# Kernel tuning notes

Hardware: AMD Instinct MI355X
Metric: run time of the kernel (lower is better)

The kernel has to match this reference:

```python
import jax, jax.numpy as jnp
import numpy as np

B, S, H = 16, 512, 2048
NH, NKV = 16, 4
HD = H // NH  # 128


def _rope_tables(seq_len, dim, dtype):
    inv_freq = 1.0 / (10000.0 ** (jnp.arange(0, dim, 2, dtype=jnp.float32) / dim))
    t = jnp.arange(seq_len, dtype=jnp.float32)
    freqs = jnp.einsum('i,j->ij', t, inv_freq)          # [S, HD/2]
    emb = jnp.concatenate([freqs, freqs], axis=-1)       # [S, HD]
    cos = jnp.cos(emb)[None, None].astype(dtype)         # [1,1,S,HD]
    sin = jnp.sin(emb)[None, None].astype(dtype)
    return cos, sin


def _rotate_half(x):
    x1, x2 = jnp.split(x, 2, axis=-1)
    return jnp.concatenate([-x2, x1], axis=-1)


def setup_inputs() -> dict:
    key = jax.random.key(0)
    kx, kq, kk, kv, ko = jax.random.split(key, 5)
    x = jax.random.normal(kx, (B, S, H), dtype=jnp.float32)
    s = 0.02
    Wq = jax.random.normal(kq, (H, H), dtype=jnp.float32) * s
    Wk = jax.random.normal(kk, (NKV * HD, H), dtype=jnp.float32) * s
    Wv = jax.random.normal(kv, (NKV * HD, H), dtype=jnp.float32) * s
    Wo = jax.random.normal(ko, (H, H), dtype=jnp.float32) * s
    return {"x": x, "Wq": Wq, "Wk": Wk, "Wv": Wv, "Wo": Wo}


def reference(x, Wq, Wk, Wv, Wo):
    b, s, _ = x.shape
    scaling = HD ** -0.5
    # projections (torch Linear: y = x @ W.T, W is [out,in])
    q = jnp.einsum('bsh,oh->bso', x, Wq).reshape(b, s, NH, HD).transpose(0, 2, 1, 3)
    k = jnp.einsum('bsh,oh->bso', x, Wk).reshape(b, s, NKV, HD).transpose(0, 2, 1, 3)
    v = jnp.einsum('bsh,oh->bso', x, Wv).reshape(b, s, NKV, HD).transpose(0, 2, 1, 3)
    cos, sin = _rope_tables(s, HD, x.dtype)
    q = q * cos + _rotate_half(q) * sin
    k = k * cos + _rotate_half(k) * sin
    rep = NH // NKV
    k = jnp.repeat(k, rep, axis=1)  # [b, NH, s, HD]
    v = jnp.repeat(v, rep, axis=1)
    scores = jnp.einsum('bhqd,bhkd->bhqk', q, k) * scaling
    attn = jax.nn.softmax(scores, axis=-1)
    out = jnp.einsum('bhqk,bhkd->bhqd', attn, v)
    out = out.transpose(0, 2, 1, 3).reshape(b, s, H)
    return jnp.einsum('bsh,oh->bso', out, Wo)
```

## Files before the change

### kernel.cpp

```cpp
#include <hip/hip_runtime.h>
#include <stdint.h>


typedef _Float16 f16;
typedef _Float16 f16x4 __attribute__((ext_vector_type(4)));
typedef _Float16 f16x8 __attribute__((ext_vector_type(8)));
typedef float f32x4 __attribute__((ext_vector_type(4)));

#define B_   16
#define S_   512
#define H_   2048
#define NH_  16
#define NKV_ 4
#define HD_  128
#define ATT_SCALE 0.08838834764831843f
#define LOG2_10000_DIV64 0.20762050593045952f

#define AS1 __attribute__((address_space(1)))
#define AS3 __attribute__((address_space(3)))

__device__ __forceinline__ void async16(const void* g, const void* l) {
  __builtin_amdgcn_global_load_lds((const AS1 unsigned int*)(uintptr_t)g,
                                   (AS3 unsigned int*)(uintptr_t)l, 16, 0, 0);
}

__global__ __launch_bounds__(256) void cast_all(const float* __restrict__ x,
                                                const float* __restrict__ wq,
                                                const float* __restrict__ wk,
                                                const float* __restrict__ wv,
                                                const float* __restrict__ wo,
                                                f16* __restrict__ x_h,
                                                f16* __restrict__ w_h,
                                                f16* __restrict__ wo_h) {
  const int i = blockIdx.x * 256 + threadIdx.x;
  const float4* src;
  f16x4* dst;
  if (i < 4194304) {
    src = (const float4*)x + i;            dst = (f16x4*)x_h + i;
  } else if (i < 5242880) {
    int j = i - 4194304;
    src = (const float4*)wq + j;           dst = (f16x4*)w_h + j;
  } else if (i < 5505024) {
    int j = i - 5242880;
    src = (const float4*)wk + j;           dst = (f16x4*)w_h + 1048576 + j;
  } else if (i < 5767168) {
    int j = i - 5505024;
    src = (const float4*)wv + j;           dst = (f16x4*)w_h + 1310720 + j;
  } else {
    int j = i - 5767168;
    src = (const float4*)wo + j;           dst = (f16x4*)wo_h + j;
  }
  float4 v = *src;
  f16x4 o = {(f16)v.x, (f16)v.y, (f16)v.z, (f16)v.w};
  *dst = o;
}

template<int MODE>
__global__ __launch_bounds__(512, 2) void gemm_k(const f16* __restrict__ A,
                                                 const f16* __restrict__ W,
                                                 f16* __restrict__ qo,
                                                 f16* __restrict__ ko,
                                                 f16* __restrict__ vto,
                                                 float* __restrict__ fout) {
  __shared__ __align__(16) f16 As[3][256 * 64];
  __shared__ __align__(16) f16 Bs[3][128 * 64];
  const int K = 2048;
  const int NT = 32;
  const int m0 = blockIdx.x * 256;
  const int n0 = blockIdx.y * 128;
  const int tid = threadIdx.x;
  const int wave = tid >> 6, lane = tid & 63;
  const int quad = lane >> 4, l15 = lane & 15;
  const int wm = wave >> 1, wn = wave & 1;

  const f16* aptr[4];
  const f16* bptr[2];
#pragma unroll
  for (int i = 0; i < 4; ++i) {
    const int L = i * 512 + wave * 64 + lane;
    const int r = L >> 3, s = L & 7;
    aptr[i] = A + (size_t)(m0 + r) * K + (s ^ (r & 7)) * 8;
  }
#pragma unroll
  for (int i = 0; i < 2; ++i) {
    const int L = i * 512 + wave * 64 + lane;
    const int r = L >> 3, s = L & 7;
    bptr[i] = W + (size_t)(n0 + r) * K + (s ^ (r & 7)) * 8;
  }
  const int ldsw = wave * 1024;

  f32x4 acc[4][4] = {};
  f16x8 aC[4], bC[4], aN[4], bN[4];

  auto ldA = [&](f16x8* d, const f16* base, int ks) {
#pragma unroll
    for (int mi = 0; mi < 4; ++mi) {
      const int row = wm * 64 + mi * 16 + l15;
      const int slot = (ks * 4 + quad) ^ (l15 & 7);
      d[mi] = *reinterpret_cast<const f16x8*>(base + row * 64 + slot * 8);
    }
  };
  auto ldB = [&](f16x8* d, const f16* base, int ks) {
#pragma unroll
    for (int ni = 0; ni < 4; ++ni) {
      const int col = wn * 32 + (ni >> 1) * 64 + (ni & 1) * 16 + l15;
      const int slot = (ks * 4 + quad) ^ (l15 & 7);
      d[ni] = *reinterpret_cast<const f16x8*>(base + col * 64 + slot * 8);
    }
  };
  auto mfma16 = [&](const f16x8* Af, const f16x8* Bf) {
#pragma unroll
    for (int mi = 0; mi < 4; ++mi)
#pragma unroll
      for (int ni = 0; ni < 4; ++ni)
        acc[mi][ni] = __builtin_amdgcn_mfma_f32_16x16x32_f16(Af[mi], Bf[ni], acc[mi][ni], 0, 0, 0);
  };

#pragma unroll
  for (int t = 0; t < 2; ++t) {
#pragma unroll
    for (int i = 0; i < 4; ++i)
      async16(aptr[i] + t * 64, (const char*)&As[t][0] + i * 8192 + ldsw);
#pragma unroll
    for (int i = 0; i < 2; ++i)
      async16(bptr[i] + t * 64, (const char*)&Bs[t][0] + i * 8192 + ldsw);
  }
  asm volatile("s_waitcnt vmcnt(6)" ::: "memory");
  __builtin_amdgcn_s_barrier();
  ldA(aC, &As[0][0], 0);
  ldB(bC, &Bs[0][0], 0);

  for (int t = 0; t < NT; ++t) {
    const int buf = t % 3, bufn = (t + 1) % 3, bufs = (t + 2) % 3;
    const int sk = (t + 2) * 64;

    ldA(aN, &As[buf][0], 1);
    ldB(bN, &Bs[buf][0], 1);
    if (t + 2 < NT) {
      async16(aptr[0] + sk, (const char*)&As[bufs][0] + 0 * 8192 + ldsw);
      async16(aptr[1] + sk, (const char*)&As[bufs][0] + 1 * 8192 + ldsw);
      async16(bptr[0] + sk, (const char*)&Bs[bufs][0] + 0 * 8192 + ldsw);
    }
    asm volatile("s_waitcnt lgkmcnt(8)" ::: "memory");
    __builtin_amdgcn_sched_barrier(0);
    __builtin_amdgcn_s_setprio(1);
    mfma16(aC, bC);
    __builtin_amdgcn_s_setprio(0);

    if (t + 1 < NT) {
      if (t + 2 < NT) asm volatile("s_waitcnt vmcnt(3)" ::: "memory");
      else            asm volatile("s_waitcnt vmcnt(0)" ::: "memory");
      __builtin_amdgcn_s_barrier();
    }

    if (t + 1 < NT) {
      ldA(aC, &As[bufn][0], 0);
      ldB(bC, &Bs[bufn][0], 0);
    }
    if (t + 2 < NT) {
      async16(aptr[2] + sk, (const char*)&As[bufs][0] + 2 * 8192 + ldsw);
      async16(aptr[3] + sk, (const char*)&As[bufs][0] + 3 * 8192 + ldsw);
      async16(bptr[1] + sk, (const char*)&Bs[bufs][0] + 1 * 8192 + ldsw);
    }
    if (t + 1 < NT) asm volatile("s_waitcnt lgkmcnt(8)" ::: "memory");
    else            asm volatile("s_waitcnt lgkmcnt(0)" ::: "memory");
    __builtin_amdgcn_sched_barrier(0);
    __builtin_amdgcn_s_setprio(1);
    mfma16(aN, bN);
    __builtin_amdgcn_s_setprio(0);
    if (t + 1 < NT) __builtin_amdgcn_s_barrier();
  }

  if constexpr (MODE == 1) {
    const int b_ = m0 >> 9;
    if (n0 >= 2560) {
      const int h = (n0 - 2560) >> 7;
      f16* vb = vto + ((size_t)b_ * NKV_ + h) * HD_ * S_;
#pragma unroll
      for (int mi = 0; mi < 4; ++mi)
#pragma unroll
        for (int r = 0; r < 4; ++r) {
          const int s = (m0 + wm * 64 + mi * 16 + quad * 4 + r) & 511;
#pragma unroll
          for (int ni = 0; ni < 4; ++ni) {
            const int d = (ni >> 1) * 64 + wn * 32 + (ni & 1) * 16 + l15;
            vb[(size_t)d * S_ + s] = (f16)acc[mi][ni][r];
          }
        }
    } else {
      f16* ob = (n0 < 2048)
          ? (qo + ((size_t)b_ * NH_ + (n0 >> 7)) * S_ * HD_)
          : (ko + ((size_t)b_ * NKV_ + ((n0 - 2048) >> 7)) * S_ * HD_);
      float invf[2];
#pragma unroll
      for (int ni = 0; ni < 2; ++ni)
        invf[ni] = exp2f((float)(wn * 32 + ni * 16 + l15) * -LOG2_10000_DIV64);
#pragma unroll
      for (int mi = 0; mi < 4; ++mi)
#pragma unroll
        for (int r = 0; r < 4; ++r) {
          const int s = (m0 + wm * 64 + mi * 16 + quad * 4 + r) & 511;
          const size_t rb = (size_t)s * HD_;
#pragma unroll
          for (int ni = 0; ni < 2; ++ni) {
            const int d = wn * 32 + ni * 16 + l15;
            float sn, cs;
            __sincosf((float)s * invf[ni], &sn, &cs);
            const float x1 = acc[mi][ni][r], x2 = acc[mi][ni + 2][r];
            ob[rb + d] = (f16)(x1 * cs - x2 * sn);
            ob[rb + d + 64] = (f16)(x2 * cs + x1 * sn);
          }
        }
    }
  } else {
#pragma unroll
    for (int mi = 0; mi < 4; ++mi)
#pragma unroll
      for (int ni = 0; ni < 4; ++ni) {
        const int ncol = n0 + wn * 32 + (ni >> 1) * 64 + (ni & 1) * 16 + l15;
#pragma unroll
        for (int r = 0; r < 4; ++r) {
          const int mrow = m0 + wm * 64 + mi * 16 + quad * 4 + r;
          fout[(size_t)mrow * 2048 + ncol] = acc[mi][ni][r];
        }
      }
  }
}

__global__ __launch_bounds__(512) void attn_kernel(const f16* __restrict__ q,
                                                   const f16* __restrict__ k,
                                                   const f16* __restrict__ vt,
                                                   f16* __restrict__ out) {
  __shared__ __align__(16) f16 Qs[128 * 128];
  __shared__ __align__(16) f16 Ks[128 * 128];
  __shared__ __align__(16) f16 Vs[128 * 128];
  __shared__ __align__(16) f16 Ps[8][16 * 136];

  const int qt = blockIdx.x, h = blockIdx.y, b = blockIdx.z;
  const int kvh = h >> 2;
  const int tid = threadIdx.x;
  const int wave = tid >> 6, lane = tid & 63;
  const int quad = lane >> 4, l15 = lane & 15;
  const int sm0 = wave * 16;

  const f16* qbase = q + (((size_t)b * NH_ + h) * S_ + qt * 128) * HD_;
  const f16* kbase = k + ((size_t)b * NKV_ + kvh) * S_ * HD_;
  const f16* vbase = vt + ((size_t)b * NKV_ + kvh) * HD_ * S_;

#pragma unroll
  for (int i = 0; i < 4; ++i) {
    const int L = wave * 256 + i * 64 + lane;
    const int r = L >> 4;
    const int c = (L & 15) ^ (r & 15);
    async16(qbase + (size_t)r * HD_ + c * 8, (const char*)Qs + (size_t)(wave * 256 + i * 64) * 16);
  }

  f32x4 O[8] = {};
  float mrun[4], lrun[4];
#pragma unroll
  for (int r = 0; r < 4; ++r) { mrun[r] = -3.0e38f; lrun[r] = 0.f; }

  for (int j = 0; j < 4; ++j) {
    if (j) __syncthreads();
#pragma unroll
    for (int i = 0; i < 4; ++i) {
      const int L = wave * 256 + i * 64 + lane;
      const int r = L >> 4;
      const int c = (L & 15) ^ (r & 15);
      async16(kbase + (size_t)(j * 128 + r) * HD_ + c * 8,
              (const char*)Ks + (size_t)(wave * 256 + i * 64) * 16);
      async16(vbase + (size_t)r * S_ + j * 128 + c * 8,
              (const char*)Vs + (size_t)(wave * 256 + i * 64) * 16);
    }
    __syncthreads();

    f32x4 Sc[8] = {};
#pragma unroll
    for (int ks = 0; ks < 4; ++ks) {
      f16x8 aq, bk[8];
      aq = *reinterpret_cast<const f16x8*>(Qs + ((sm0 + l15) * 16 + (((ks * 4 + quad) ^ l15))) * 8);
#pragma unroll
      for (int ni = 0; ni < 8; ++ni)
        bk[ni] = *reinterpret_cast<const f16x8*>(Ks + ((ni * 16 + l15) * 16 + ((ks * 4 + quad) ^ l15)) * 8);
#pragma unroll
      for (int ni = 0; ni < 8; ++ni)
        Sc[ni] = __builtin_amdgcn_mfma_f32_16x16x32_f16(aq, bk[ni], Sc[ni], 0, 0, 0);
    }

#pragma unroll
    for (int r = 0; r < 4; ++r) {
      float mx = -3.0e38f;
#pragma unroll
      for (int ni = 0; ni < 8; ++ni) mx = fmaxf(mx, Sc[ni][r]);
      mx *= ATT_SCALE;
#pragma unroll
      for (int off = 1; off < 16; off <<= 1) mx = fmaxf(mx, __shfl_xor(mx, off));
      const float mnew = fmaxf(mrun[r], mx);
      const float alpha = __expf(mrun[r] - mnew);
      float rs = 0.f;
#pragma unroll
      for (int ni = 0; ni < 8; ++ni) {
        const float pv = __expf(Sc[ni][r] * ATT_SCALE - mnew);
        Sc[ni][r] = pv;
        rs += pv;
      }
#pragma unroll
      for (int off = 1; off < 16; off <<= 1) rs += __shfl_xor(rs, off);
      lrun[r] = lrun[r] * alpha + rs;
      mrun[r] = mnew;
#pragma unroll
      for (int ni = 0; ni < 8; ++ni) O[ni][r] *= alpha;
#pragma unroll
      for (int ni = 0; ni < 8; ++ni)
        Ps[wave][(quad * 4 + r) * 136 + ni * 16 + l15] = (f16)Sc[ni][r];
    }

#pragma unroll
    for (int ks = 0; ks < 4; ++ks) {
      f16x8 ap, bv[8];
      ap = *reinterpret_cast<const f16x8*>(&Ps[wave][l15 * 136 + ks * 32 + quad * 8]);
#pragma unroll
      for (int ni = 0; ni < 8; ++ni)
        bv[ni] = *reinterpret_cast<const f16x8*>(Vs + ((ni * 16 + l15) * 16 + ((ks * 4 + quad) ^ l15)) * 8);
#pragma unroll
      for (int ni = 0; ni < 8; ++ni)
        O[ni] = __builtin_amdgcn_mfma_f32_16x16x32_f16(ap, bv[ni], O[ni], 0, 0, 0);
    }
  }

#pragma unroll
  for (int r = 0; r < 4; ++r) {
    const float inv = 1.f / lrun[r];
    const int srow = qt * 128 + sm0 + quad * 4 + r;
#pragma unroll
    for (int ni = 0; ni < 8; ++ni)
      out[((size_t)b * S_ + srow) * H_ + h * HD_ + ni * 16 + l15] = (f16)(O[ni][r] * inv);
  }
}

extern "C" void kernel_launch(void* const* d_in, const int* in_sizes, int n_in,
                              void* d_out, int out_size, void* d_ws, size_t ws_size,
                              hipStream_t stream) {
  const float* x = (const float*)d_in[0];
  const float* Wq = (const float*)d_in[1];
  const float* Wk = (const float*)d_in[2];
  const float* Wv = (const float*)d_in[3];
  const float* Wo = (const float*)d_in[4];
  float* out = (float*)d_out;
  char* ws = (char*)d_ws;

  f16* x_h  = (f16*)(ws + 0);
  f16* w_h  = (f16*)(ws + 33554432);
  f16* wo_h = (f16*)(ws + 46137344);
  f16* qb   = (f16*)(ws + 54525952);
  f16* kb   = (f16*)(ws + 88080384);
  f16* vtb  = (f16*)(ws + 96468992);
  f16* attn = (f16*)(ws + 104857600);

  cast_all<<<26624, 256, 0, stream>>>(x, Wq, Wk, Wv, Wo, x_h, w_h, wo_h);
  gemm_k<1><<<dim3(32, 24), 512, 0, stream>>>(x_h, w_h, qb, kb, vtb, nullptr);
  attn_kernel<<<dim3(4, 16, 16), 512, 0, stream>>>(qb, kb, vtb, attn);
  gemm_k<0><<<dim3(32, 16), 512, 0, stream>>>(attn, wo_h, nullptr, nullptr, nullptr, out);
}
```

Measured before the change: 381.7 us.

## Restructure attention with 256-row Q tiles, register Q, double-buffered K staging

The attention kernel now gives each block 256 query rows (32 per wave), keeping Q fragments in registers instead of LDS. It steps over 64-key chunks, double-buffers K and overlaps the V load with the QK^T compute, and the K load for the next chunk with the PV compute. LDS shrinks and launch_bounds asks for 4 blocks per CU, so K/V traffic per query drops and occupancy can rise. The cost is twice as many loop iterations, more sync points, and fewer blocks in the grid (512 instead of 1024), which may hurt load balance across CUs.

```diff
diff --git a/kernel.cpp b/kernel.cpp
--- a/kernel.cpp
+++ b/kernel.cpp
@@ -227,115 +227,153 @@
   }
 }
 
-__global__ __launch_bounds__(512) void attn_kernel(const f16* __restrict__ q,
-                                                   const f16* __restrict__ k,
-                                                   const f16* __restrict__ vt,
-                                                   f16* __restrict__ out) {
-  __shared__ __align__(16) f16 Qs[128 * 128];
-  __shared__ __align__(16) f16 Ks[128 * 128];
-  __shared__ __align__(16) f16 Vs[128 * 128];
-  __shared__ __align__(16) f16 Ps[8][16 * 136];
+__global__ __launch_bounds__(512, 4) void attn_kernel(const f16* __restrict__ q,
+                                                      const f16* __restrict__ k,
+                                                      const f16* __restrict__ vt,
+                                                      f16* __restrict__ out) {
+  __shared__ __align__(16) f16 Kb[2][64 * 128];
+  __shared__ __align__(16) f16 Vb[128 * 64];
+  __shared__ __align__(16) f16 Ps[8][32 * 64];
 
   const int qt = blockIdx.x, h = blockIdx.y, b = blockIdx.z;
   const int kvh = h >> 2;
   const int tid = threadIdx.x;
   const int wave = tid >> 6, lane = tid & 63;
   const int quad = lane >> 4, l15 = lane & 15;
-  const int sm0 = wave * 16;
-
-  const f16* qbase = q + (((size_t)b * NH_ + h) * S_ + qt * 128) * HD_;
+
+  const f16* qbase = q + (((size_t)b * NH_ + h) * S_ + qt * 256) * HD_;
   const f16* kbase = k + ((size_t)b * NKV_ + kvh) * S_ * HD_;
   const f16* vbase = vt + ((size_t)b * NKV_ + kvh) * HD_ * S_;
 
-#pragma unroll
-  for (int i = 0; i < 4; ++i) {
-    const int L = wave * 256 + i * 64 + lane;
-    const int r = L >> 4;
-    const int c = (L & 15) ^ (r & 15);
-    async16(qbase + (size_t)r * HD_ + c * 8, (const char*)Qs + (size_t)(wave * 256 + i * 64) * 16);
-  }
-
-  f32x4 O[8] = {};
-  float mrun[4], lrun[4];
-#pragma unroll
-  for (int r = 0; r < 4; ++r) { mrun[r] = -3.0e38f; lrun[r] = 0.f; }
-
-  for (int j = 0; j < 4; ++j) {
-    if (j) __syncthreads();
-#pragma unroll
-    for (int i = 0; i < 4; ++i) {
-      const int L = wave * 256 + i * 64 + lane;
-      const int r = L >> 4;
-      const int c = (L & 15) ^ (r & 15);
-      async16(kbase + (size_t)(j * 128 + r) * HD_ + c * 8,
-              (const char*)Ks + (size_t)(wave * 256 + i * 64) * 16);
-      async16(vbase + (size_t)r * S_ + j * 128 + c * 8,
-              (const char*)Vs + (size_t)(wave * 256 + i * 64) * 16);
-    }
-    __syncthreads();
-
-    f32x4 Sc[8] = {};
+  auto stageK = [&](int j) {
+    f16* dst = &Kb[j & 1][0];
+#pragma unroll
+    for (int i = 0; i < 2; ++i) {
+      const int L0 = i * 512 + wave * 64;
+      const int L = L0 + lane;
+      const int r = L >> 4, c = L & 15;
+      async16(kbase + (size_t)(j * 64 + r) * HD_ + (c ^ (r & 15)) * 8,
+              (const char*)dst + (size_t)L0 * 16);
+    }
+  };
+  auto stageV = [&](int j) {
+#pragma unroll
+    for (int i = 0; i < 2; ++i) {
+      const int L0 = i * 512 + wave * 64;
+      const int L = L0 + lane;
+      const int r = L >> 3, c = L & 7;
+      async16(vbase + (size_t)r * S_ + j * 64 + (c ^ (r & 7)) * 8,
+              (const char*)&Vb[0] + (size_t)L0 * 16);
+    }
+  };
+
+  f16x8 aq[2][4];
+#pragma unroll
+  for (int mi = 0; mi < 2; ++mi)
+#pragma unroll
+    for (int ks = 0; ks < 4; ++ks)
+      aq[mi][ks] = *reinterpret_cast<const f16x8*>(
+          qbase + (size_t)(wave * 32 + mi * 16 + l15) * HD_ + ks * 32 + quad * 8);
+
+  stageK(0);
+
+  f32x4 O[2][8] = {};
+  float mrun[2][4], lrun[2][4];
+#pragma unroll
+  for (int mi = 0; mi < 2; ++mi)
+#pragma unroll
+    for (int r = 0; r < 4; ++r) { mrun[mi][r] = -3.0e38f; lrun[mi][r] = 0.f; }
+
+  for (int j = 0; j < 8; ++j) {
+    asm volatile("s_waitcnt vmcnt(0)" ::: "memory");
+    __builtin_amdgcn_s_barrier();
+    stageV(j);
+
+    f32x4 Sc[2][4] = {};
 #pragma unroll
     for (int ks = 0; ks < 4; ++ks) {
-      f16x8 aq, bk[8];
-      aq = *reinterpret_cast<const f16x8*>(Qs + ((sm0 + l15) * 16 + (((ks * 4 + quad) ^ l15))) * 8);
+      f16x8 bk[4];
+#pragma unroll
+      for (int ni = 0; ni < 4; ++ni) {
+        const int row = ni * 16 + l15;
+        bk[ni] = *reinterpret_cast<const f16x8*>(
+            &Kb[j & 1][row * 128 + (((ks * 4 + quad) ^ l15) & 15) * 8]);
+      }
+#pragma unroll
+      for (int mi = 0; mi < 2; ++mi)
+#pragma unroll
+        for (int ni = 0; ni < 4; ++ni)
+          Sc[mi][ni] = __builtin_amdgcn_mfma_f32_16x16x32_f16(aq[mi][ks], bk[ni], Sc[mi][ni], 0, 0, 0);
+    }
+
+#pragma unroll
+    for (int mi = 0; mi < 2; ++mi)
+#pragma unroll
+      for (int r = 0; r < 4; ++r) {
+        float mx = fmaxf(fmaxf(Sc[mi][0][r], Sc[mi][1][r]),
+                         fmaxf(Sc[mi][2][r], Sc[mi][3][r]));
+        mx *= ATT_SCALE;
+#pragma unroll
+        for (int off = 1; off < 16; off <<= 1) mx = fmaxf(mx, __shfl_xor(mx, off));
+        const float mnew = fmaxf(mrun[mi][r], mx);
+        const float alpha = __expf(mrun[mi][r] - mnew);
+        float rs = 0.f;
+#pragma unroll
+        for (int ni = 0; ni < 4; ++ni) {
+          const float pv = __expf(Sc[mi][ni][r] * ATT_SCALE - mnew);
+          Sc[mi][ni][r] = pv;
+          rs += pv;
+        }
+#pragma unroll
+        for (int off = 1; off < 16; off <<= 1) rs += __shfl_xor(rs, off);
+        lrun[mi][r] = lrun[mi][r] * alpha + rs;
+        mrun[mi][r] = mnew;
+#pragma unroll
+        for (int ni = 0; ni < 8; ++ni) O[mi][ni][r] *= alpha;
+        const int rowl = mi * 16 + quad * 4 + r;
+#pragma unroll
+        for (int ni = 0; ni < 4; ++ni) {
+          const int col = ni * 16 + l15;
+          Ps[wave][rowl * 64 + (((ni * 2 + (l15 >> 3)) ^ (rowl & 7)) << 3) + (l15 & 7)] =
+              (f16)Sc[mi][ni][r];
+        }
+      }
+
+    asm volatile("s_waitcnt vmcnt(0)" ::: "memory");
+    __builtin_amdgcn_s_barrier();
+    if (j < 7) stageK(j + 1);
+
+#pragma unroll
+    for (int ks = 0; ks < 2; ++ks) {
+      f16x8 ap[2];
+#pragma unroll
+      for (int mi = 0; mi < 2; ++mi) {
+        const int rowl = mi * 16 + l15;
+        ap[mi] = *reinterpret_cast<const f16x8*>(
+            &Ps[wave][rowl * 64 + (((ks * 4 + quad) ^ (l15 & 7)) << 3)]);
+      }
+#pragma unroll
+      for (int ni = 0; ni < 8; ++ni) {
+        const int row = ni * 16 + l15;
+        const f16x8 bv = *reinterpret_cast<const f16x8*>(
+            &Vb[row * 64 + (((ks * 4 + quad) ^ (l15 & 7)) << 3)]);
+#pragma unroll
+        for (int mi = 0; mi < 2; ++mi)
+          O[mi][ni] = __builtin_amdgcn_mfma_f32_16x16x32_f16(ap[mi], bv, O[mi][ni], 0, 0, 0);
+      }
+    }
+  }
+
+#pragma unroll
+  for (int mi = 0; mi < 2; ++mi)
+#pragma unroll
+    for (int r = 0; r < 4; ++r) {
+      const float inv = 1.f / lrun[mi][r];
+      const int srow = qt * 256 + wave * 32 + mi * 16 + quad * 4 + r;
 #pragma unroll
       for (int ni = 0; ni < 8; ++ni)
-        bk[ni] = *reinterpret_cast<const f16x8*>(Ks + ((ni * 16 + l15) * 16 + ((ks * 4 + quad) ^ l15)) * 8);
-#pragma unroll
-      for (int ni = 0; ni < 8; ++ni)
-        Sc[ni] = __builtin_amdgcn_mfma_f32_16x16x32_f16(aq, bk[ni], Sc[ni], 0, 0, 0);
-    }
-
-#pragma unroll
-    for (int r = 0; r < 4; ++r) {
-      float mx = -3.0e38f;
-#pragma unroll
-      for (int ni = 0; ni < 8; ++ni) mx = fmaxf(mx, Sc[ni][r]);
-      mx *= ATT_SCALE;
-#pragma unroll
-      for (int off = 1; off < 16; off <<= 1) mx = fmaxf(mx, __shfl_xor(mx, off));
-      const float mnew = fmaxf(mrun[r], mx);
-      const float alpha = __expf(mrun[r] - mnew);
-      float rs = 0.f;
-#pragma unroll
-      for (int ni = 0; ni < 8; ++ni) {
-        const float pv = __expf(Sc[ni][r] * ATT_SCALE - mnew);
-        Sc[ni][r] = pv;
-        rs += pv;
-      }
-#pragma unroll
-      for (int off = 1; off < 16; off <<= 1) rs += __shfl_xor(rs, off);
-      lrun[r] = lrun[r] * alpha + rs;
-      mrun[r] = mnew;
-#pragma unroll
-      for (int ni = 0; ni < 8; ++ni) O[ni][r] *= alpha;
-#pragma unroll
-      for (int ni = 0; ni < 8; ++ni)
-        Ps[wave][(quad * 4 + r) * 136 + ni * 16 + l15] = (f16)Sc[ni][r];
-    }
-
-#pragma unroll
-    for (int ks = 0; ks < 4; ++ks) {
-      f16x8 ap, bv[8];
-      ap = *reinterpret_cast<const f16x8*>(&Ps[wave][l15 * 136 + ks * 32 + quad * 8]);
-#pragma unroll
-      for (int ni = 0; ni < 8; ++ni)
-        bv[ni] = *reinterpret_cast<const f16x8*>(Vs + ((ni * 16 + l15) * 16 + ((ks * 4 + quad) ^ l15)) * 8);
-#pragma unroll
-      for (int ni = 0; ni < 8; ++ni)
-        O[ni] = __builtin_amdgcn_mfma_f32_16x16x32_f16(ap, bv[ni], O[ni], 0, 0, 0);
-    }
-  }
-
-#pragma unroll
-  for (int r = 0; r < 4; ++r) {
-    const float inv = 1.f / lrun[r];
-    const int srow = qt * 128 + sm0 + quad * 4 + r;
-#pragma unroll
-    for (int ni = 0; ni < 8; ++ni)
-      out[((size_t)b * S_ + srow) * H_ + h * HD_ + ni * 16 + l15] = (f16)(O[ni][r] * inv);
-  }
+        out[((size_t)b * S_ + srow) * H_ + h * HD_ + ni * 16 + l15] = (f16)(O[mi][ni][r] * inv);
+    }
 }
 
 extern "C" void kernel_launch(void* const* d_in, const int* in_sizes, int n_in,
@@ -359,6 +397,6 @@
 
   cast_all<<<26624, 256, 0, stream>>>(x, Wq, Wk, Wv, Wo, x_h, w_h, wo_h);
   gemm_k<1><<<dim3(32, 24), 512, 0, stream>>>(x_h, w_h, qb, kb, vtb, nullptr);
-  attn_kernel<<<dim3(4, 16, 16), 512, 0, stream>>>(qb, kb, vtb, attn);
+  attn_kernel<<<dim3(2, 16, 16), 512, 0, stream>>>(qb, kb, vtb, attn);
   gemm_k<0><<<dim3(32, 16), 512, 0, stream>>>(attn, wo_h, nullptr, nullptr, nullptr, out);
 }
```

New measurement: 518.9 us. 1.36x slower.
